# Performance work log

Hardware: AMD Instinct MI355X
Metric: run time of the kernel (lower is better)

Reference implementation:

```python
import jax, jax.numpy as jnp
import numpy as np

D = 768; H = 12; DH = D // H; L = 12; FF = 3072; P = 20
IMG = (640, 360); NP_ = (IMG[0] // P) * (IMG[1] // P)  # 576 patches
NC = 10
EPS = 1e-5


def setup_inputs() -> dict:
    key = jax.random.key(0)
    ks = jax.random.split(key, 20)
    s = 0.02
    inp = {
        "x": jax.random.normal(ks[0], (16, 3, IMG[0], IMG[1]), jnp.float32),
        "patch_w": jax.random.normal(ks[1], (D, 3, P, P), jnp.float32) * s,
        "patch_b": jnp.zeros((D,), jnp.float32),
        "pos_emb": jax.random.normal(ks[2], (1, NP_, D), jnp.float32),
        "ln_g": jnp.ones((D,), jnp.float32),
        "ln_b": jnp.zeros((D,), jnp.float32),
        "Wq": jax.random.normal(ks[3], (L, D, D), jnp.float32) * s,
        "bq": jnp.zeros((L, D), jnp.float32),
        "Wk": jax.random.normal(ks[4], (L, D, D), jnp.float32) * s,
        "bk": jnp.zeros((L, D), jnp.float32),
        "Wv": jax.random.normal(ks[5], (L, D, D), jnp.float32) * s,
        "bv": jnp.zeros((L, D), jnp.float32),
        "Wo": jax.random.normal(ks[6], (L, D, D), jnp.float32) * s,
        "bo": jnp.zeros((L, D), jnp.float32),
        "W1": jax.random.normal(ks[7], (L, FF, D), jnp.float32) * s,
        "b1": jnp.zeros((L, FF), jnp.float32),
        "W2": jax.random.normal(ks[8], (L, D, FF), jnp.float32) * s,
        "b2": jnp.zeros((L, D), jnp.float32),
        "fc_w": jax.random.normal(ks[9], (NC, D), jnp.float32) * s,
        "fc_b": jnp.zeros((NC,), jnp.float32),
    }
    return inp


def _layer_norm(x, g, b):
    mu = jnp.mean(x, axis=-1, keepdims=True)
    var = jnp.mean(jnp.square(x - mu), axis=-1, keepdims=True)
    return (x - mu) * jax.lax.rsqrt(var + EPS) * g + b


def _forward(x, patch_w, patch_b, pos_emb, ln_g, ln_b,
             Wq, bq, Wk, bk, Wv, bv, Wo, bo, W1, b1, W2, b2, fc_w, fc_b):
    B = x.shape[0]
    Hp, Wp = IMG[0] // P, IMG[1] // P
    # patch embed: stride=kernel conv == per-patch linear
    patches = x.reshape(B, 3, Hp, P, Wp, P).transpose(0, 2, 4, 1, 3, 5)
    patches = patches.reshape(B, Hp * Wp, 3 * P * P)           # [B, N, 3*p*p]
    h = patches @ patch_w.reshape(D, -1).T + patch_b            # [B, N, D]
    h = h + pos_emb
    h = _layer_norm(h, ln_g, ln_b)

    def layer(h, p):
        wq, bq_, wk, bk_, wv, bv_, wo, bo_, w1, b1_, w2, b2_ = p
        N = h.shape[1]
        def heads(t):  # [B,N,D] -> [B,H,N,DH]
            return t.reshape(B, N, H, DH).transpose(0, 2, 1, 3)
        q = heads(h @ wq.T + bq_)
        k = heads(h @ wk.T + bk_)
        v = heads(h @ wv.T + bv_)
        scores = jnp.einsum('bhqd,bhkd->bhqk', q, k) / jnp.sqrt(jnp.float32(DH))
        attn = jax.nn.softmax(scores, axis=-1)
        o = jnp.einsum('bhqk,bhkd->bhqd', attn, v)
        o = o.transpose(0, 2, 1, 3).reshape(B, N, D) @ wo.T + bo_
        h = h + o
        ff = jax.nn.relu(h @ w1.T + b1_) @ w2.T + b2_
        return h + ff, None

    h, _ = jax.lax.scan(layer, h, (Wq, bq, Wk, bk, Wv, bv, Wo, bo, W1, b1, W2, b2))
    pooled = h.mean(axis=1)                                     # [B, D]
    return pooled @ fc_w.T + fc_b                               # [B, NC]


def reference(x, patch_w, patch_b, pos_emb, ln_g, ln_b,
              Wq, bq, Wk, bk, Wv, bv, Wo, bo, W1, b1, W2, b2, fc_w, fc_b):
    return _forward(x, patch_w, patch_b, pos_emb, ln_g, ln_b,
                    Wq, bq, Wk, bk, Wv, bv, Wo, bo, W1, b1, W2, b2, fc_w, fc_b)
```

## Files before the change

kernel.cpp:

```cpp
#include <hip/hip_runtime.h>
#include <stdint.h>
#include <stddef.h>

typedef __attribute__((ext_vector_type(8))) short short8;
typedef __attribute__((ext_vector_type(4))) float f32x4;
typedef __attribute__((ext_vector_type(4))) float float4v;
typedef __attribute__((ext_vector_type(4))) unsigned short us4;

#define D_    768
#define HH    12
#define DHEAD 64
#define NP    576
#define BB    16
#define MROWS 9216
#define KPAT  1216
#define SCL   0.18033688011112042f

static __device__ __forceinline__ unsigned short f2bf(float f){
  union { float f; unsigned int u; } v; v.f = f;
  unsigned int u = v.u;
  return (unsigned short)((u + 0x7FFFu + ((u >> 16) & 1u)) >> 16);
}

static __device__ __forceinline__ us4 f2bf4(float4v v){
  us4 r;
  r.x = f2bf(v.x); r.y = f2bf(v.y); r.z = f2bf(v.z); r.w = f2bf(v.w);
  return r;
}

static __device__ __forceinline__ void gld16(const void* g, void* l){
  __builtin_amdgcn_global_load_lds((const __attribute__((address_space(1))) void*)g,
                                   (__attribute__((address_space(3))) void*)l,
                                   16, 0, 0);
}

static __device__ __forceinline__ void barx(){
  asm volatile("" ::: "memory");
  __builtin_amdgcn_s_barrier();
  asm volatile("" ::: "memory");
}

__global__ __launch_bounds__(512, 4) void gemm3r(
    const unsigned short* __restrict__ A,
    const unsigned short* __restrict__ W,
    const float* __restrict__ bias,
    const float* __restrict__ pos,
    const float* res,
    float* outf,
    unsigned short* outb,
    int M, int N, int K, int relu)
{
  __shared__ unsigned short sA[3][256*32];
  __shared__ unsigned short sB[3][128*32];
  const int NB = N >> 7;
  const int nwg = (int)gridDim.x;
  const int wid0 = (int)blockIdx.x;
  const int xcd = wid0 & 7, bidx = wid0 >> 3;
  const int q = nwg >> 3, r = nwg & 7;
  const int wid = (xcd < r ? xcd*(q+1) : r*(q+1) + (xcd-r)*q) + bidx;
  const int mb = wid / NB, nb = wid % NB;
  const int m0 = mb << 8, n0 = nb << 7;
  const int t = threadIdx.x;
  const int w = t >> 6, l = t & 63;
  const int wr = w >> 1, wc = w & 1;
  const int fr = l & 15, fq = l >> 4;
  const int srow = l >> 2;
  const int schk = (l & 3) ^ ((l >> 3) & 3);

  const f32x4 zero = {0.f, 0.f, 0.f, 0.f};
  f32x4 acc[4][4];
  #pragma unroll
  for (int i = 0; i < 4; ++i)
    #pragma unroll
    for (int j = 0; j < 4; ++j) acc[i][j] = zero;

  const int P = K >> 5;

  auto stg = [&](int h){
    const int s = h % 3;
    #pragma unroll
    for (int i = 0; i < 2; ++i){
      const int rb = i*128 + w*16;
      gld16(A + (size_t)(m0 + rb + srow) * K + (h<<5) + (schk<<3), &sA[s][rb*32]);
    }
    const int rb = w*16;
    gld16(W + (size_t)(n0 + rb + srow) * K + (h<<5) + (schk<<3), &sB[s][rb*32]);
  };

  stg(0); stg(1);
  asm volatile("s_waitcnt vmcnt(3)" ::: "memory");
  barx();

  for (int p = 0; p < P; ++p){
    const int s = p % 3;
    short8 a[4], b[4];
    #pragma unroll
    for (int i = 0; i < 4; ++i){
      const int R = wr*64 + i*16 + fr;
      a[i] = *(const short8*)&sA[s][R*32 + ((fq ^ ((R>>1)&3))<<3)];
    }
    #pragma unroll
    for (int j = 0; j < 4; ++j){
      const int C = wc*64 + j*16 + fr;
      b[j] = *(const short8*)&sB[s][C*32 + ((fq ^ ((C>>1)&3))<<3)];
    }
    if (p + 2 < P) stg(p + 2);
    __builtin_amdgcn_s_setprio(1);
    #pragma unroll
    for (int i = 0; i < 4; ++i)
      #pragma unroll
      for (int j = 0; j < 4; ++j)
        acc[i][j] = __builtin_amdgcn_mfma_f32_16x16x32_bf16(a[i], b[j], acc[i][j], 0, 0, 0);
    __builtin_amdgcn_s_setprio(0);
    if (p + 1 < P){
      if (p == P - 2) asm volatile("s_waitcnt vmcnt(0)" ::: "memory");
      else            asm volatile("s_waitcnt vmcnt(3)" ::: "memory");
      barx();
    }
  }

  #pragma unroll
  for (int mf = 0; mf < 4; ++mf){
    #pragma unroll
    for (int nf = 0; nf < 4; ++nf){
      #pragma unroll
      for (int rr = 0; rr < 4; ++rr){
        const int row = m0 + wr*64 + mf*16 + (fq<<2) + rr;
        const int col = n0 + wc*64 + nf*16 + fr;
        float v = acc[mf][nf][rr] + bias[col];
        if (pos)  v += pos[(size_t)(row % NP) * D_ + col];
        if (res)  v += res[(size_t)row * N + col];
        if (relu) v = fmaxf(v, 0.f);
        const size_t idx = (size_t)row * N + col;
        if (outf) outf[idx] = v;
        if (outb) outb[idx] = f2bf(v);
      }
    }
  }
}

__global__ __launch_bounds__(512) void gemm4p(
    const unsigned short* __restrict__ A,
    const unsigned short* __restrict__ W,
    const float* __restrict__ bias,
    const float* __restrict__ pos,
    const float* res,
    float* outf,
    unsigned short* outb,
    int M, int N, int K, int relu)
{
  __shared__ unsigned short sA[4][128*32];
  __shared__ unsigned short sB[4][128*32];
  const int NB = N >> 7;
  const int nwg = (int)gridDim.x;
  const int wid0 = (int)blockIdx.x;
  const int xcd = wid0 & 7, bidx = wid0 >> 3;
  const int q = nwg >> 3, r = nwg & 7;
  const int wid = (xcd < r ? xcd*(q+1) : r*(q+1) + (xcd-r)*q) + bidx;
  const int mb = wid / NB, nb = wid % NB;
  const int m0 = mb << 7, n0 = nb << 7;
  const int t = threadIdx.x;
  const int w = t >> 6, l = t & 63;
  const int wr = w >> 1, wc = w & 1;
  const int fr = l & 15, fq = l >> 4;

  const int srow = l >> 2;
  const int schk = (l & 3) ^ ((l >> 3) & 3);

  const f32x4 zero = {0.f, 0.f, 0.f, 0.f};
  f32x4 acc[2][4];
  #pragma unroll
  for (int i = 0; i < 2; ++i)
    #pragma unroll
    for (int j = 0; j < 4; ++j) acc[i][j] = zero;

  const int P = K >> 5;

  auto stg = [&](int h){
    const int rb = w*16;
    gld16(A + (size_t)(m0 + rb + srow) * K + (h<<5) + (schk<<3), &sA[h & 3][rb*32]);
    gld16(W + (size_t)(n0 + rb + srow) * K + (h<<5) + (schk<<3), &sB[h & 3][rb*32]);
  };

  stg(0); stg(1); stg(2);
  asm volatile("s_waitcnt vmcnt(4)" ::: "memory");
  barx();

  short8 a[2], b[4];
  for (int p = 0; p < P; ++p){
    const int slot = p & 3;
    #pragma unroll
    for (int i = 0; i < 2; ++i){
      const int R = wr*32 + i*16 + fr;
      a[i] = *(const short8*)&sA[slot][R*32 + ((fq ^ ((R>>1)&3))<<3)];
    }
    #pragma unroll
    for (int i = 0; i < 4; ++i){
      const int C = wc*64 + i*16 + fr;
      b[i] = *(const short8*)&sB[slot][C*32 + ((fq ^ ((C>>1)&3))<<3)];
    }
    if (p + 3 < P) stg(p + 3);
    __builtin_amdgcn_s_setprio(1);
    #pragma unroll
    for (int i = 0; i < 2; ++i)
      #pragma unroll
      for (int j = 0; j < 4; ++j)
        acc[i][j] = __builtin_amdgcn_mfma_f32_16x16x32_bf16(a[i], b[j], acc[i][j], 0, 0, 0);
    __builtin_amdgcn_s_setprio(0);
    if (p + 1 < P){
      if      (p <= P - 4) asm volatile("s_waitcnt vmcnt(4)" ::: "memory");
      else if (p == P - 3) asm volatile("s_waitcnt vmcnt(2)" ::: "memory");
      else                 asm volatile("s_waitcnt vmcnt(0)" ::: "memory");
      barx();
    }
  }

  #pragma unroll
  for (int mf = 0; mf < 2; ++mf){
    #pragma unroll
    for (int nf = 0; nf < 4; ++nf){
      #pragma unroll
      for (int rr = 0; rr < 4; ++rr){
        const int row = m0 + wr*32 + mf*16 + (fq<<2) + rr;
        const int col = n0 + wc*64 + nf*16 + fr;
        float v = acc[mf][nf][rr] + bias[col];
        if (pos)  v += pos[(size_t)(row % NP) * D_ + col];
        if (res)  v += res[(size_t)row * N + col];
        if (relu) v = fmaxf(v, 0.f);
        const size_t idx = (size_t)row * N + col;
        if (outf) outf[idx] = v;
        if (outb) outb[idx] = f2bf(v);
      }
    }
  }
}

__global__ __launch_bounds__(384) void k_attn(const unsigned short* __restrict__ qkv,
                                              unsigned short* __restrict__ o)
{
  __shared__ unsigned short Kl[2][32*64];
  __shared__ unsigned short Vt[2][64*64];
  const int nwg = (int)gridDim.x;
  int wid = (int)blockIdx.x;
  wid = (wid & 7) * (nwg >> 3) + (wid >> 3);
  const int bh = wid / 3, qs = wid % 3;
  const int b = bh / HH, h = bh % HH;
  const unsigned short* base = qkv + (size_t)b * NP * 2304 + h * DHEAD;
  const int t = threadIdx.x;
  const int w = t >> 6, l = t & 63;
  const int fr = l & 15, fq = l >> 4;
  const int sg = l & 7;
  const int sr = ((w & 3) << 3) + (l >> 3);
  const bool stw = (t < 256);

  short8 qfa[2], qfb[2];
  #pragma unroll
  for (int qt = 0; qt < 2; ++qt){
    const size_t qrow = (size_t)(qs*192 + (qt*6 + w)*16 + fr);
    qfa[qt] = *(const short8*)(base + qrow*2304 + (fq<<3));
    qfb[qt] = *(const short8*)(base + qrow*2304 + 32 + (fq<<3));
  }

  const f32x4 zero = {0.f, 0.f, 0.f, 0.f};
  float mx_[2] = {-1e30f, -1e30f};
  float ls_[2] = {0.f, 0.f};
  f32x4 oa[2][4];
  #pragma unroll
  for (int qt = 0; qt < 2; ++qt)
    #pragma unroll
    for (int nf = 0; nf < 4; ++nf) oa[qt][nf] = zero;

  if (stw){
    gld16(base + 768 + (size_t)sr*2304 + ((sg ^ (sr&7))<<3), &Kl[0][(w&3)*512]);
    short8 vv = *(const short8*)(base + 1536 + (size_t)sr*2304 + (sg<<3));
    asm volatile("s_waitcnt vmcnt(0)" ::: "memory");
    #pragma unroll
    for (int j = 0; j < 8; ++j){
      const int d = sg*8 + j;
      const int off = (d<<7) + ((((sr>>3) ^ j ^ sg) & 7) << 4) + ((sr&7)<<1);
      *(unsigned short*)((char*)&Vt[0][0] + off) = ((const unsigned short*)&vv)[j];
    }
  }
  __syncthreads();

  for (int kt = 0; kt < 18; ++kt){
    const int buf = kt & 1;
    short8 vv;
    const bool st = stw && (kt < 17);
    if (st){
      const int key = (kt+1)*32 + sr;
      gld16(base + 768 + (size_t)key*2304 + ((sg ^ (sr&7))<<3), &Kl[buf^1][(w&3)*512]);
      vv = *(const short8*)(base + 1536 + (size_t)key*2304 + (sg<<3));
    }

    const char* kb = (const char*)&Kl[buf][0];
    const int r0 = fr, r1 = 16 + fr;
    const short8 k00 = *(const short8*)(kb + (r0<<7) + (((fq    ) ^ (r0&7))<<4));
    const short8 k01 = *(const short8*)(kb + (r0<<7) + (((4+fq ) ^ (r0&7))<<4));
    const short8 k10 = *(const short8*)(kb + (r1<<7) + (((fq    ) ^ (r1&7))<<4));
    const short8 k11 = *(const short8*)(kb + (r1<<7) + (((4+fq ) ^ (r1&7))<<4));
    const char* vb = (const char*)&Vt[buf][0];

    #pragma unroll
    for (int qt = 0; qt < 2; ++qt){
      f32x4 s0 = zero, s1 = zero;
      s0 = __builtin_amdgcn_mfma_f32_16x16x32_bf16(k00, qfa[qt], s0, 0, 0, 0);
      s0 = __builtin_amdgcn_mfma_f32_16x16x32_bf16(k01, qfb[qt], s0, 0, 0, 0);
      s1 = __builtin_amdgcn_mfma_f32_16x16x32_bf16(k10, qfa[qt], s1, 0, 0, 0);
      s1 = __builtin_amdgcn_mfma_f32_16x16x32_bf16(k11, qfb[qt], s1, 0, 0, 0);
      float mx = fmaxf(fmaxf(fmaxf(s0[0], s0[1]), fmaxf(s0[2], s0[3])),
                       fmaxf(fmaxf(s1[0], s1[1]), fmaxf(s1[2], s1[3])));
      mx = fmaxf(mx, __shfl_xor(mx, 16));
      mx = fmaxf(mx, __shfl_xor(mx, 32));
      const float mn = fmaxf(mx_[qt], mx * SCL);
      const float fc = exp2f(mx_[qt] - mn);
      const float p0 = exp2f(s0[0]*SCL - mn), p1 = exp2f(s0[1]*SCL - mn);
      const float p2 = exp2f(s0[2]*SCL - mn), p3 = exp2f(s0[3]*SCL - mn);
      const float p4 = exp2f(s1[0]*SCL - mn), p5 = exp2f(s1[1]*SCL - mn);
      const float p6 = exp2f(s1[2]*SCL - mn), p7 = exp2f(s1[3]*SCL - mn);
      float ps = ((p0+p1)+(p2+p3)) + ((p4+p5)+(p6+p7));
      ps += __shfl_xor(ps, 16);
      ps += __shfl_xor(ps, 32);
      ls_[qt] = ls_[qt] * fc + ps;
      mx_[qt] = mn;
      if (!__all(fc == 1.0f)){
        const float fA = __shfl(fc, (fq<<2) + 0);
        const float fB = __shfl(fc, (fq<<2) + 1);
        const float fC = __shfl(fc, (fq<<2) + 2);
        const float fD = __shfl(fc, (fq<<2) + 3);
        #pragma unroll
        for (int nf = 0; nf < 4; ++nf){
          oa[qt][nf][0] *= fA; oa[qt][nf][1] *= fB;
          oa[qt][nf][2] *= fC; oa[qt][nf][3] *= fD;
        }
      }
      unsigned d0, d1, d2, d3;
      asm("v_cvt_pk_bf16_f32 %0, %1, %2" : "=v"(d0) : "v"(p0), "v"(p1));
      asm("v_cvt_pk_bf16_f32 %0, %1, %2" : "=v"(d1) : "v"(p2), "v"(p3));
      asm("v_cvt_pk_bf16_f32 %0, %1, %2" : "=v"(d2) : "v"(p4), "v"(p5));
      asm("v_cvt_pk_bf16_f32 %0, %1, %2" : "=v"(d3) : "v"(p6), "v"(p7));
      const int srcA = fr + ((fq & 1) << 5);
      const unsigned a0 = (unsigned)__shfl((int)d0, srcA);
      const unsigned a1 = (unsigned)__shfl((int)d1, srcA);
      const unsigned a2 = (unsigned)__shfl((int)d2, srcA);
      const unsigned a3 = (unsigned)__shfl((int)d3, srcA);
      const unsigned b0 = (unsigned)__shfl((int)d0, srcA + 16);
      const unsigned b1 = (unsigned)__shfl((int)d1, srcA + 16);
      const unsigned b2 = (unsigned)__shfl((int)d2, srcA + 16);
      const unsigned b3 = (unsigned)__shfl((int)d3, srcA + 16);
      const bool hi = fq >= 2;
      union { unsigned u[4]; short8 v; } pk;
      pk.u[0] = hi ? a2 : a0;
      pk.u[1] = hi ? a3 : a1;
      pk.u[2] = hi ? b2 : b0;
      pk.u[3] = hi ? b3 : b1;
      const short8 pa = pk.v;
      #pragma unroll
      for (int nf = 0; nf < 4; ++nf){
        const int d = (nf<<4) + fr;
        const short8 vf = *(const short8*)(vb + (d<<7) + (((fq ^ (d&7) ^ (d>>3)) & 7)<<4));
        oa[qt][nf] = __builtin_amdgcn_mfma_f32_16x16x32_bf16(pa, vf, oa[qt][nf], 0, 0, 0);
      }
    }

    if (st){
      asm volatile("s_waitcnt vmcnt(0)" ::: "memory");
      #pragma unroll
      for (int j = 0; j < 8; ++j){
        const int d = sg*8 + j;
        const int off = (d<<7) + ((((sr>>3) ^ j ^ sg) & 7) << 4) + ((sr&7)<<1);
        *(unsigned short*)((char*)&Vt[buf^1][0] + off) = ((const unsigned short*)&vv)[j];
      }
    }
    __syncthreads();
  }

  #pragma unroll
  for (int qt = 0; qt < 2; ++qt){
    const float rl = 1.f / ls_[qt];
    const float rA = __shfl(rl, (fq<<2)+0), rB = __shfl(rl, (fq<<2)+1);
    const float rC = __shfl(rl, (fq<<2)+2), rD = __shfl(rl, (fq<<2)+3);
    const size_t r0 = (size_t)(b*NP + qs*192 + (qt*6 + w)*16 + (fq<<2));
    #pragma unroll
    for (int nf = 0; nf < 4; ++nf){
      const int col = h*DHEAD + (nf<<4) + fr;
      o[(r0 + 0)*D_ + col] = f2bf(oa[qt][nf][0] * rA);
      o[(r0 + 1)*D_ + col] = f2bf(oa[qt][nf][1] * rB);
      o[(r0 + 2)*D_ + col] = f2bf(oa[qt][nf][2] * rC);
      o[(r0 + 3)*D_ + col] = f2bf(oa[qt][nf][3] * rD);
    }
  }
}

__global__ void k_wconv(const float* __restrict__ Wq, const float* __restrict__ Wk,
                        const float* __restrict__ Wv, const float* __restrict__ Wo,
                        const float* __restrict__ W1, const float* __restrict__ W2,
                        unsigned short* __restrict__ wqkv, unsigned short* __restrict__ wo,
                        unsigned short* __restrict__ w1, unsigned short* __restrict__ w2){
  const long Q4 = 5308416, O4 = 1769472, F4 = 7077888;
  const long n4 = Q4 + O4 + F4 + F4;
  long i = (long)blockIdx.x * blockDim.x + threadIdx.x;
  const long st = (long)gridDim.x * blockDim.x;
  for (; i < n4; i += st){
    if (i < Q4){
      const int lay = (int)(i / (2304 * 192));
      const int rem = (int)(i % (2304 * 192));
      const int r = rem / 192, k4 = rem % 192;
      const float* s = (r < 768) ? Wq : ((r < 1536) ? Wk : Wv);
      const int rr = (r < 768) ? r : ((r < 1536) ? r - 768 : r - 1536);
      ((us4*)wqkv)[i] = f2bf4(*(const float4v*)(s + (size_t)lay * 589824 + (size_t)rr * 768 + k4*4));
    } else if (i < Q4 + O4){
      const long j = i - Q4;
      ((us4*)wo)[j] = f2bf4(((const float4v*)Wo)[j]);
    } else if (i < Q4 + O4 + F4){
      const long j = i - Q4 - O4;
      ((us4*)w1)[j] = f2bf4(((const float4v*)W1)[j]);
    } else {
      const long j = i - Q4 - O4 - F4;
      ((us4*)w2)[j] = f2bf4(((const float4v*)W2)[j]);
    }
  }
}

__global__ void k_pack_qkvb(const float* __restrict__ bq, const float* __restrict__ bk,
                            const float* __restrict__ bv, float* __restrict__ dst){
  const int i = blockIdx.x * 256 + threadIdx.x;
  if (i >= 12 * 2304) return;
  const int lay = i / 2304, r = i % 2304;
  const float* s = (r < 768) ? bq : ((r < 1536) ? bk : bv);
  const int rr = (r < 768) ? r : ((r < 1536) ? r - 768 : r - 1536);
  dst[i] = s[lay * 768 + rr];
}

__global__ void k_patchw(const float* __restrict__ s, unsigned short* __restrict__ d){
  const long n4 = (long)768 * (KPAT/4);
  long i = (long)blockIdx.x * blockDim.x + threadIdx.x;
  const long st = (long)gridDim.x * blockDim.x;
  for (; i < n4; i += st){
    const int r = (int)(i / (KPAT/4)), k4 = (int)(i % (KPAT/4));
    us4 o = {0,0,0,0};
    if (k4*4 < 1200)
      o = f2bf4(*(const float4v*)(s + (size_t)r * 1200 + k4*4));
    ((us4*)d)[i] = o;
  }
}

__global__ void k_patches(const float* __restrict__ x, unsigned short* __restrict__ d){
  const long n4 = (long)MROWS * (KPAT/4);
  long i = (long)blockIdx.x * blockDim.x + threadIdx.x;
  const long st = (long)gridDim.x * blockDim.x;
  for (; i < n4; i += st){
    const int mrow = (int)(i / (KPAT/4)), k4 = (int)(i % (KPAT/4));
    const int k = k4 * 4;
    us4 o = {0,0,0,0};
    if (k < 1200){
      const int c = k / 400, rem = k % 400, py = rem / 20, px = rem % 20;
      const int b = mrow / NP, pn = mrow % NP, hp = pn / 18, wp = pn % 18;
      const float4v v = *(const float4v*)(x + ((((size_t)b * 3 + c) * 640 + hp * 20 + py) * 360 + wp * 20 + px));
      o = f2bf4(v);
    }
    ((us4*)d)[i] = o;
  }
}

__global__ __launch_bounds__(256) void k_ln(float* h, unsigned short* hb,
                                            const float* __restrict__ g,
                                            const float* __restrict__ bt){
  const int r = blockIdx.x, t = threadIdx.x;
  const size_t base = (size_t)r * D_;
  const float x0 = h[base + t], x1 = h[base + t + 256], x2 = h[base + t + 512];
  float s = x0 + x1 + x2;
  #pragma unroll
  for (int o = 1; o < 64; o <<= 1) s += __shfl_xor(s, o);
  __shared__ float red[8];
  const int w = t >> 6, l = t & 63;
  if (l == 0) red[w] = s;
  __syncthreads();
  const float mu = (red[0] + red[1] + red[2] + red[3]) * (1.f / 768.f);
  const float d0 = x0 - mu, d1 = x1 - mu, d2 = x2 - mu;
  float v = d0*d0 + d1*d1 + d2*d2;
  #pragma unroll
  for (int o = 1; o < 64; o <<= 1) v += __shfl_xor(v, o);
  if (l == 0) red[4 + w] = v;
  __syncthreads();
  const float var = (red[4] + red[5] + red[6] + red[7]) * (1.f / 768.f);
  const float rs = rsqrtf(var + 1e-5f);
  const float y0 = d0 * rs * g[t]       + bt[t];
  const float y1 = d1 * rs * g[t + 256] + bt[t + 256];
  const float y2 = d2 * rs * g[t + 512] + bt[t + 512];
  h[base + t] = y0; h[base + t + 256] = y1; h[base + t + 512] = y2;
  hb[base + t] = f2bf(y0); hb[base + t + 256] = f2bf(y1); hb[base + t + 512] = f2bf(y2);
}

__global__ void k_pool(const float* __restrict__ h, float* __restrict__ p){
  const int i = blockIdx.x * 256 + threadIdx.x;
  const int b = i / D_, c = i % D_;
  const float* base = h + (size_t)b * NP * D_ + c;
  float s = 0.f;
  for (int n = 0; n < NP; ++n) s += base[(size_t)n * D_];
  p[i] = s * (1.f / 576.f);
}

__global__ __launch_bounds__(64) void k_fc(const float* __restrict__ p, const float* __restrict__ w,
                                           const float* __restrict__ bias, float* __restrict__ out){
  const int oi = blockIdx.x;
  const int b = oi / 10, j = oi % 10;
  const int l = threadIdx.x;
  float s = 0.f;
  for (int c = l; c < D_; c += 64) s += p[b * D_ + c] * w[j * D_ + c];
  #pragma unroll
  for (int o = 1; o < 64; o <<= 1) s += __shfl_xor(s, o);
  if (l == 0) out[oi] = s + bias[j];
}

extern "C" void kernel_launch(void* const* d_in, const int* in_sizes, int n_in,
                              void* d_out, int out_size, void* d_ws, size_t ws_size,
                              hipStream_t stream)
{
  const float* x       = (const float*)d_in[0];
  const float* patch_w = (const float*)d_in[1];
  const float* patch_b = (const float*)d_in[2];
  const float* pos_emb = (const float*)d_in[3];
  const float* ln_g    = (const float*)d_in[4];
  const float* ln_b    = (const float*)d_in[5];
  const float* Wq      = (const float*)d_in[6];
  const float* bq      = (const float*)d_in[7];
  const float* Wk      = (const float*)d_in[8];
  const float* bk      = (const float*)d_in[9];
  const float* Wv      = (const float*)d_in[10];
  const float* bv      = (const float*)d_in[11];
  const float* Wo      = (const float*)d_in[12];
  const float* bo      = (const float*)d_in[13];
  const float* W1      = (const float*)d_in[14];
  const float* b1      = (const float*)d_in[15];
  const float* W2      = (const float*)d_in[16];
  const float* b2      = (const float*)d_in[17];
  const float* fc_w    = (const float*)d_in[18];
  const float* fc_b    = (const float*)d_in[19];
  float* out = (float*)d_out;
  (void)in_sizes; (void)n_in; (void)out_size; (void)ws_size;

  char* ws = (char*)d_ws;
  size_t off = 0;
  auto alloc = [&](size_t bytes) -> char* {
    char* p = ws + off;
    off += (bytes + 255) & ~(size_t)255;
    return p;
  };
  unsigned short* wqkv    = (unsigned short*)alloc((size_t)12*2304*768*2);
  unsigned short* wo      = (unsigned short*)alloc((size_t)12*768*768*2);
  unsigned short* w1      = (unsigned short*)alloc((size_t)12*3072*768*2);
  unsigned short* w2      = (unsigned short*)alloc((size_t)12*768*3072*2);
  unsigned short* wp      = (unsigned short*)alloc((size_t)768*KPAT*2);
  float*          bqkv    = (float*)alloc((size_t)12*2304*4);
  unsigned short* patches = (unsigned short*)alloc((size_t)MROWS*KPAT*2);
  float*          hf      = (float*)alloc((size_t)MROWS*D_*4);
  unsigned short* hb      = (unsigned short*)alloc((size_t)MROWS*D_*2);
  unsigned short* qkvb    = (unsigned short*)alloc((size_t)MROWS*2304*2);
  unsigned short* ob      = (unsigned short*)alloc((size_t)MROWS*D_*2);
  unsigned short* ffb     = (unsigned short*)alloc((size_t)MROWS*3072*2);
  float*          pooled  = (float*)alloc((size_t)16*D_*4);

  k_wconv<<<2048, 256, 0, stream>>>(Wq, Wk, Wv, Wo, W1, W2, wqkv, wo, w1, w2);
  k_pack_qkvb<<<(12*2304 + 255)/256, 256, 0, stream>>>(bq, bk, bv, bqkv);
  k_patchw<<<2048, 256, 0, stream>>>(patch_w, wp);
  k_patches<<<2048, 256, 0, stream>>>(x, patches);

  gemm4p<<<72*6, 512, 0, stream>>>(patches, wp, patch_b, pos_emb,
                                   nullptr, hf, nullptr, MROWS, 768, KPAT, 0);
  k_ln<<<MROWS, 256, 0, stream>>>(hf, hb, ln_g, ln_b);

  for (int l = 0; l < 12; ++l){
    gemm3r<<<36*18, 512, 0, stream>>>(hb, wqkv + (size_t)l*2304*768, bqkv + l*2304,
                                      nullptr, nullptr, nullptr, qkvb, MROWS, 2304, 768, 0);
    k_attn<<<576, 384, 0, stream>>>(qkvb, ob);
    gemm4p<<<72*6, 512, 0, stream>>>(ob, wo + (size_t)l*768*768, bo + l*768,
                                     nullptr, hf, hf, hb, MROWS, 768, 768, 0);
    gemm3r<<<36*24, 512, 0, stream>>>(hb, w1 + (size_t)l*3072*768, b1 + (size_t)l*3072,
                                      nullptr, nullptr, nullptr, ffb, MROWS, 3072, 768, 1);
    gemm4p<<<72*6, 512, 0, stream>>>(ffb, w2 + (size_t)l*768*3072, b2 + l*768,
                                     nullptr, hf, hf, hb, MROWS, 768, 3072, 0);
  }
  k_pool<<<48, 256, 0, stream>>>(hf, pooled);
  k_fc<<<160, 64, 0, stream>>>(pooled, fc_w, fc_b, out);
}
```

Measured before the change: 3.508 ms.

## Deepen N=768 GEMM LDS pipeline to five stages, two K-steps per barrier

Measured after the change: 3.576 ms. About the same (+1.9%).

```diff
diff --git a/kernel.cpp b/kernel.cpp
--- a/kernel.cpp
+++ b/kernel.cpp
@@ -139,7 +139,7 @@
   }
 }
 
-__global__ __launch_bounds__(512) void gemm4p(
+__global__ __launch_bounds__(512, 4) void gemm5p(
     const unsigned short* __restrict__ A,
     const unsigned short* __restrict__ W,
     const float* __restrict__ bias,
@@ -149,8 +149,8 @@
     unsigned short* outb,
     int M, int N, int K, int relu)
 {
-  __shared__ unsigned short sA[4][128*32];
-  __shared__ unsigned short sB[4][128*32];
+  __shared__ unsigned short sA[5][128*32];
+  __shared__ unsigned short sB[5][128*32];
   const int NB = N >> 7;
   const int nwg = (int)gridDim.x;
   const int wid0 = (int)blockIdx.x;
@@ -177,40 +177,53 @@
   const int P = K >> 5;
 
   auto stg = [&](int h){
+    const int s = h % 5;
     const int rb = w*16;
-    gld16(A + (size_t)(m0 + rb + srow) * K + (h<<5) + (schk<<3), &sA[h & 3][rb*32]);
-    gld16(W + (size_t)(n0 + rb + srow) * K + (h<<5) + (schk<<3), &sB[h & 3][rb*32]);
+    gld16(A + (size_t)(m0 + rb + srow) * K + (h<<5) + (schk<<3), &sA[s][rb*32]);
+    gld16(W + (size_t)(n0 + rb + srow) * K + (h<<5) + (schk<<3), &sB[s][rb*32]);
   };
 
   stg(0); stg(1); stg(2);
-  asm volatile("s_waitcnt vmcnt(4)" ::: "memory");
+  asm volatile("s_waitcnt vmcnt(2)" ::: "memory");
   barx();
 
-  short8 a[2], b[4];
-  for (int p = 0; p < P; ++p){
-    const int slot = p & 3;
+  const int IT = P >> 1;
+  for (int it = 0; it < IT; ++it){
+    const int h0 = 2*it;
+    const int s0 = h0 % 5, s1 = (h0+1) % 5;
+    short8 a0[2], b0[4], a1[2], b1[4];
     #pragma unroll
     for (int i = 0; i < 2; ++i){
       const int R = wr*32 + i*16 + fr;
-      a[i] = *(const short8*)&sA[slot][R*32 + ((fq ^ ((R>>1)&3))<<3)];
-    }
-    #pragma unroll
-    for (int i = 0; i < 4; ++i){
-      const int C = wc*64 + i*16 + fr;
-      b[i] = *(const short8*)&sB[slot][C*32 + ((fq ^ ((C>>1)&3))<<3)];
-    }
-    if (p + 3 < P) stg(p + 3);
+      const int o = R*32 + ((fq ^ ((R>>1)&3))<<3);
+      a0[i] = *(const short8*)&sA[s0][o];
+      a1[i] = *(const short8*)&sA[s1][o];
+    }
+    #pragma unroll
+    for (int j = 0; j < 4; ++j){
+      const int C = wc*64 + j*16 + fr;
+      const int o = C*32 + ((fq ^ ((C>>1)&3))<<3);
+      b0[j] = *(const short8*)&sB[s0][o];
+      b1[j] = *(const short8*)&sB[s1][o];
+    }
+    const bool g3 = (h0 + 3) < P, g4 = (h0 + 4) < P;
+    if (g3) stg(h0 + 3);
+    if (g4) stg(h0 + 4);
     __builtin_amdgcn_s_setprio(1);
     #pragma unroll
     for (int i = 0; i < 2; ++i)
       #pragma unroll
       for (int j = 0; j < 4; ++j)
-        acc[i][j] = __builtin_amdgcn_mfma_f32_16x16x32_bf16(a[i], b[j], acc[i][j], 0, 0, 0);
+        acc[i][j] = __builtin_amdgcn_mfma_f32_16x16x32_bf16(a0[i], b0[j], acc[i][j], 0, 0, 0);
+    #pragma unroll
+    for (int i = 0; i < 2; ++i)
+      #pragma unroll
+      for (int j = 0; j < 4; ++j)
+        acc[i][j] = __builtin_amdgcn_mfma_f32_16x16x32_bf16(a1[i], b1[j], acc[i][j], 0, 0, 0);
     __builtin_amdgcn_s_setprio(0);
-    if (p + 1 < P){
-      if      (p <= P - 4) asm volatile("s_waitcnt vmcnt(4)" ::: "memory");
-      else if (p == P - 3) asm volatile("s_waitcnt vmcnt(2)" ::: "memory");
-      else                 asm volatile("s_waitcnt vmcnt(0)" ::: "memory");
+    if (it + 1 < IT){
+      if (g4) asm volatile("s_waitcnt vmcnt(2)" ::: "memory");
+      else    asm volatile("s_waitcnt vmcnt(0)" ::: "memory");
       barx();
     }
   }
@@ -561,12 +574,12 @@
   unsigned short* ffb     = (unsigned short*)alloc((size_t)MROWS*3072*2);
   float*          pooled  = (float*)alloc((size_t)16*D_*4);
 
-  k_wconv<<<2048, 256, 0, stream>>>(Wq, Wk, Wv, Wo, W1, W2, wqkv, wo, w1, w2);
+  k_wconv<<<8192, 256, 0, stream>>>(Wq, Wk, Wv, Wo, W1, W2, wqkv, wo, w1, w2);
   k_pack_qkvb<<<(12*2304 + 255)/256, 256, 0, stream>>>(bq, bk, bv, bqkv);
   k_patchw<<<2048, 256, 0, stream>>>(patch_w, wp);
   k_patches<<<2048, 256, 0, stream>>>(x, patches);
 
-  gemm4p<<<72*6, 512, 0, stream>>>(patches, wp, patch_b, pos_emb,
+  gemm5p<<<72*6, 512, 0, stream>>>(patches, wp, patch_b, pos_emb,
                                    nullptr, hf, nullptr, MROWS, 768, KPAT, 0);
   k_ln<<<MROWS, 256, 0, stream>>>(hf, hb, ln_g, ln_b);
 
@@ -574,11 +587,11 @@
     gemm3r<<<36*18, 512, 0, stream>>>(hb, wqkv + (size_t)l*2304*768, bqkv + l*2304,
                                       nullptr, nullptr, nullptr, qkvb, MROWS, 2304, 768, 0);
     k_attn<<<576, 384, 0, stream>>>(qkvb, ob);
-    gemm4p<<<72*6, 512, 0, stream>>>(ob, wo + (size_t)l*768*768, bo + l*768,
+    gemm5p<<<72*6, 512, 0, stream>>>(ob, wo + (size_t)l*768*768, bo + l*768,
                                      nullptr, hf, hf, hb, MROWS, 768, 768, 0);
     gemm3r<<<36*24, 512, 0, stream>>>(hb, w1 + (size_t)l*3072*768, b1 + (size_t)l*3072,
                                       nullptr, nullptr, nullptr, ffb, MROWS, 3072, 768, 1);
-    gemm4p<<<72*6, 512, 0, stream>>>(ffb, w2 + (size_t)l*768*3072, b2 + l*768,
+    gemm5p<<<72*6, 512, 0, stream>>>(ffb, w2 + (size_t)l*768*3072, b2 + l*768,
                                      nullptr, hf, hf, hb, MROWS, 768, 3072, 0);
   }
   k_pool<<<48, 256, 0, stream>>>(hf, pooled);
```
